# Kernel tuning notes

Hardware: AMD Instinct MI355X
Metric: run time of the kernel (lower is better)

## Reference

```python
import jax, jax.numpy as jnp
import numpy as np

B = 8
A = 180      # num_angles
D = 512      # det_count
IMG = 512    # img_size


def _forward(x):
    # --- Ram-Lak filter in frequency domain ---
    freq = jnp.abs(jnp.fft.rfftfreq(D)).astype(jnp.float32)            # [D//2+1]
    filtered = jnp.fft.irfft(jnp.fft.rfft(x, axis=-1) * freq, n=D, axis=-1)  # [B,A,D]

    # --- precompute per-angle detector coordinates for every pixel ---
    lin = jnp.linspace(-1.0, 1.0, IMG, dtype=jnp.float32)
    yy, xx = jnp.meshgrid(lin, lin, indexing='ij')
    xxf = xx.reshape(-1)                                               # [HW]
    yyf = yy.reshape(-1)
    angles = jnp.linspace(0.0, np.pi - np.pi / A, A, dtype=jnp.float32)
    t = (xxf[None, :] * jnp.cos(angles)[:, None]
         + yyf[None, :] * jnp.sin(angles)[:, None]) / np.sqrt(2.0)     # [A,HW]
    u = jnp.clip((t + 1.0) * 0.5 * (D - 1.0), 0.0, D - 1.0)
    idx0 = jnp.floor(u).astype(jnp.int32)
    idx1 = jnp.minimum(idx0 + 1, D - 1)
    w = u - idx0.astype(jnp.float32)

    # --- backprojection sweep: scan over angles, accumulate in-register ---
    proj = jnp.transpose(filtered, (1, 0, 2))                          # [A,B,D]

    def step(acc, inputs):
        p, i0, i1, wa = inputs                                         # p:[B,D], i*/wa:[HW]
        s = jnp.take(p, i0, axis=1) * (1.0 - wa) + jnp.take(p, i1, axis=1) * wa
        return acc + s, None

    bn = x.shape[0]
    acc0 = jnp.zeros((bn, IMG * IMG), dtype=jnp.float32)
    acc, _ = jax.lax.scan(step, acc0, (proj, idx0, idx1, w))

    det_pixel_size = 2.0 / float(D)
    fbp = acc.reshape(bn, 1, IMG, IMG) * (det_pixel_size * np.pi / float(A))

    # --- 3x3 gaussian blur (sigma=0.5), depthwise on single channel ---
    coords = jnp.arange(-1, 2, dtype=jnp.float32)
    k1 = jnp.exp(-0.5 * (coords / 0.5) ** 2)
    k1 = k1 / k1.sum()
    k2 = jnp.outer(k1, k1)[None, None]                                 # [1,1,3,3] OIHW
    fbp = jax.lax.conv_general_dilated(fbp, k2, (1, 1), 'SAME')
    return jnp.clip(fbp, -1.0, 1.0)


def setup_inputs() -> dict:
    key = jax.random.key(0)
    x = jax.random.normal(key, (B, A, D), dtype=jnp.float32)
    return {"x": x, "input_is_sinogram": 1}


def reference(x, input_is_sinogram):
    # input_is_sinogram is a constant flag (True path): x is the sinogram [B,A,D].
    return _forward(x)
```

## Files before the change

kernel.cpp:

```cpp
#include <hip/hip_runtime.h>
#include <hip/hip_fp16.h>
#include <math.h>

#define NDET 512
#define NANG 180
#define NB   8
#define NIMG 512

#define WS_CASA 0
#define WS_CBT  360
#define WS_FGA  46440
#define WS_FGB  (46440 + 368640)
#define WS_BP   (46440 + 737280)

typedef _Float16 h2_t __attribute__((ext_vector_type(2)));

__device__ __forceinline__ void gld_lds16(const void* g, void* l) {
    __builtin_amdgcn_global_load_lds((__attribute__((address_space(1))) void*)g,
                                     (__attribute__((address_space(3))) void*)l,
                                     16, 0, 0);
}

__device__ __forceinline__ int hswz(int s) {
    return (s & 0x78) | ((s ^ (s >> 3)) & 7);
}

__global__ __launch_bounds__(512) void k_filter(const float* __restrict__ x, float* ws) {
    __shared__ float xs[8 * 516];
    __shared__ float hrs[512];
    __shared__ float fsm[512 * 8];
    const int a    = blockIdx.x;
    const int tid  = threadIdx.x;
    const int lane = tid & 63;
    const int wv   = tid >> 6;

    {
        int n = tid;
        float h;
        if (n == 0) h = 0.25f;
        else if ((n & 1) == 0) h = 0.0f;
        else {
            int m = min(n, 512 - n);
            float s = __sinf((float)m * (float)(M_PI / 512.0));
            h = -1.0f / (262144.0f * s * s);
        }
        hrs[hswz(n >> 2) * 4 + (n & 3)] = h;
    }
    {
        const float* xr = x + (wv * NANG + a) * NDET;
        float* xd = xs + wv * 516;
        *(float4*)(xd + lane * 4)       = *(const float4*)(xr + lane * 4);
        *(float4*)(xd + 256 + lane * 4) = *(const float4*)(xr + 256 + lane * 4);
    }
    if (tid == 0) {
        double th = (double)a * (M_PI / 180.0);
        double sc = 255.5 / sqrt(2.0);
        ws[WS_CASA + 2 * a]     = (float)(cos(th) * sc);
        ws[WS_CASA + 2 * a + 1] = (float)(sin(th) * sc);
    }
    if (tid < 256) {
        double th = (double)a * (M_PI / 180.0);
        double sc = 255.5 / sqrt(2.0);
        const float cad = (float)(cos(th) * sc), sad = (float)(sin(th) * sc);
        const int bx = tid & 15, by = tid >> 4;
        const float x0 = -1.f + (float)(bx * 32)      * (2.f / 511.f);
        const float x1 = -1.f + (float)(bx * 32 + 31) * (2.f / 511.f);
        const float y0 = -1.f + (float)(by * 32)      * (2.f / 511.f);
        const float y1 = -1.f + (float)(by * 32 + 31) * (2.f / 511.f);
        float u00 = fmaf(x0, cad, fmaf(y0, sad, 255.5f));
        float u01 = fmaf(x1, cad, fmaf(y0, sad, 255.5f));
        float u10 = fmaf(x0, cad, fmaf(y1, sad, 255.5f));
        float u11 = fmaf(x1, cad, fmaf(y1, sad, 255.5f));
        float umin = fminf(fminf(u00, u01), fminf(u10, u11));
        int d0 = (int)floorf(umin);
        d0 = max(0, min(NDET - 34, d0));
        ws[WS_CBT + tid * 180 + a] = 255.5f - (float)d0;
    }
    __syncthreads();

    {
        const int b  = lane & 7;
        const int t  = lane >> 3;
        const int n0 = wv * 64 + t * 8;
        const int q  = n0 >> 2;
        const float* xrow = xs + b * 516;

        float acc[8] = {0, 0, 0, 0, 0, 0, 0, 0};
        float win[12];
        {
            int s2 = (-q - 2) & 127;
            int s1 = (-q - 1) & 127;
            float4 h2 = *(const float4*)(hrs + hswz(s2) * 4);
            float4 h1 = *(const float4*)(hrs + hswz(s1) * 4);
            win[0] = h2.x; win[1] = h2.y; win[2]  = h2.z; win[3]  = h2.w;
            win[4] = h1.x; win[5] = h1.y; win[6]  = h1.z; win[7]  = h1.w;
        }
        #pragma unroll 2
        for (int c = 0; c < 128; ++c) {
            int s = (c - q) & 127;
            float4 hc = *(const float4*)(hrs + hswz(s) * 4);
            win[8] = hc.x; win[9] = hc.y; win[10] = hc.z; win[11] = hc.w;
            float4 xv = *(const float4*)(xrow + c * 4);
            float xa[4] = {xv.x, xv.y, xv.z, xv.w};
            #pragma unroll
            for (int k = 0; k < 8; ++k)
                #pragma unroll
                for (int j = 0; j < 4; ++j)
                    acc[k] = fmaf(xa[j], win[8 + j - k], acc[k]);
            #pragma unroll
            for (int i2 = 0; i2 < 8; ++i2) win[i2] = win[i2 + 4];
        }
        #pragma unroll
        for (int k = 0; k < 8; ++k)
            fsm[(n0 + k) * 8 + b] = acc[k];
    }
    __syncthreads();
    {
        const int d  = tid;
        const int d1 = min(d + 1, NDET - 1);
        const float* A  = fsm + d * 8;
        const float* Bv = fsm + d1 * 8;
        uint4 eA, eB;
        unsigned wds[8];
        #pragma unroll
        for (int b = 0; b < 8; ++b) {
            __half2 h;
            h.x = __float2half(A[b]);
            h.y = __float2half(Bv[b]);
            wds[b] = __builtin_bit_cast(unsigned, h);
        }
        eA.x = wds[0]; eA.y = wds[1]; eA.z = wds[2]; eA.w = wds[3];
        eB.x = wds[4]; eB.y = wds[5]; eB.z = wds[6]; eB.w = wds[7];
        *(uint4*)((char*)(ws + WS_FGA) + (a * NDET + d) * 16) = eA;
        *(uint4*)((char*)(ws + WS_FGB) + (a * NDET + d) * 16) = eB;
    }
}

#define WWE  33
#define CHA  60
#define ECH  (CHA * WWE)

__global__ __launch_bounds__(1024, 4) void k_bp(float* ws) {
    __shared__ uint4 win4[2][2 * ECH];
    __shared__ float casal[2 * NANG];
    __shared__ float cbl[NANG];
    const int tid  = threadIdx.x;
    const int wv   = tid >> 6, lane = tid & 63;
    const int tile = blockIdx.x;
    const int bx   = tile & 15, by = tile >> 4;
    const int iy   = by * 32 + (wv >> 2) * 8 + (lane >> 3);
    const int ix   = bx * 32 + (wv & 3) * 8 + (lane & 7);
    const float xf = -1.0f + (float)ix * (2.0f / 511.0f);
    const float yf = -1.0f + (float)iy * (2.0f / 511.0f);

    const char* __restrict__ fga = (const char*)(ws + WS_FGA);
    const char* __restrict__ fgb = (const char*)(ws + WS_FGB);

    if (tid < NANG) {
        cbl[tid] = ws[WS_CBT + tile * 180 + tid];
        casal[2 * tid]     = ws[WS_CASA + 2 * tid];
        casal[2 * tid + 1] = ws[WS_CASA + 2 * tid + 1];
    }
    __syncthreads();

    auto stageq = [&](int buf, int ch) {
        #pragma unroll
        for (int r = 0; r < 4; ++r) {
            int c = r * 1024 + tid;
            if (c < 2 * ECH) {
                int reg = c / ECH;
                int e   = c - reg * ECH;
                int a   = e / 33;
                int o   = e - a * 33;
                int ag  = ch * CHA + a;
                int d0  = (int)(255.5f - cbl[ag]);
                const char* g = (reg ? fgb : fga) + (ag * NDET + d0 + o) * 16;
                gld_lds16(g, (char*)(&win4[buf][0]) + c * 16);
            }
        }
    };

    float acc[8] = {0, 0, 0, 0, 0, 0, 0, 0};
    auto comp = [&](int buf, int ch) {
        #pragma unroll 4
        for (int al = 0; al < CHA; ++al) {
            const int ag = ch * CHA + al;
            const float ca = casal[2 * ag], sa = casal[2 * ag + 1];
            const float cb = cbl[ag];
            float v = fmaf(xf, ca, fmaf(yf, sa, cb));
            v = __builtin_amdgcn_fmed3f(v, 0.0f, 32.99996948f);
            float fj = floorf(v);
            float w  = v - fj;
            int  j0  = (int)fj;
            uint4 dA = win4[buf][al * WWE + j0];
            uint4 dB = win4[buf][ECH + al * WWE + j0];
            h2_t wp = __builtin_bit_cast(h2_t, __builtin_amdgcn_cvt_pkrtz(1.0f - w, w));
            acc[0] = __builtin_amdgcn_fdot2(__builtin_bit_cast(h2_t, dA.x), wp, acc[0], false);
            acc[1] = __builtin_amdgcn_fdot2(__builtin_bit_cast(h2_t, dA.y), wp, acc[1], false);
            acc[2] = __builtin_amdgcn_fdot2(__builtin_bit_cast(h2_t, dA.z), wp, acc[2], false);
            acc[3] = __builtin_amdgcn_fdot2(__builtin_bit_cast(h2_t, dA.w), wp, acc[3], false);
            acc[4] = __builtin_amdgcn_fdot2(__builtin_bit_cast(h2_t, dB.x), wp, acc[4], false);
            acc[5] = __builtin_amdgcn_fdot2(__builtin_bit_cast(h2_t, dB.y), wp, acc[5], false);
            acc[6] = __builtin_amdgcn_fdot2(__builtin_bit_cast(h2_t, dB.z), wp, acc[6], false);
            acc[7] = __builtin_amdgcn_fdot2(__builtin_bit_cast(h2_t, dB.w), wp, acc[7], false);
        }
    };

    stageq(0, 0); __syncthreads();
    stageq(1, 1); comp(0, 0); __syncthreads();
    stageq(0, 2); comp(1, 1); __syncthreads();
    comp(0, 2);

    const float scale = (float)((2.0 / 512.0) * M_PI / 180.0);
    float* bp = ws + WS_BP;
    #pragma unroll
    for (int b = 0; b < 8; ++b)
        bp[b * (NIMG * NIMG) + iy * NIMG + ix] = acc[b] * scale;
}

__global__ __launch_bounds__(256) void k_blur(const float* __restrict__ ws, float* __restrict__ out) {
    const int gid = blockIdx.x * 256 + threadIdx.x;
    const int b  = gid >> 18;
    const int r  = (gid >> 9) & 511;
    const int cx = gid & 511;
    const float KA = 0.10650697891920077f;
    const float KB = 0.78698604216159850f;
    const float* img = ws + WS_BP + b * (NIMG * NIMG);
    const float* rp = img + r * 512 + cx;

    float rowm = 0.0f, row0, rowp = 0.0f;
    {
        float l  = (cx > 0)   ? rp[-1] : 0.0f;
        float rr = (cx < 511) ? rp[1]  : 0.0f;
        row0 = KA * (l + rr) + KB * rp[0];
    }
    if (r > 0) {
        const float* q = rp - 512;
        float l  = (cx > 0)   ? q[-1] : 0.0f;
        float rr = (cx < 511) ? q[1]  : 0.0f;
        rowm = KA * (l + rr) + KB * q[0];
    }
    if (r < 511) {
        const float* q = rp + 512;
        float l  = (cx > 0)   ? q[-1] : 0.0f;
        float rr = (cx < 511) ? q[1]  : 0.0f;
        rowp = KA * (l + rr) + KB * q[0];
    }
    float v = KA * (rowm + rowp) + KB * row0;
    v = fminf(fmaxf(v, -1.0f), 1.0f);
    out[gid] = v;
}

extern "C" void kernel_launch(void* const* d_in, const int* in_sizes, int n_in,
                              void* d_out, int out_size, void* d_ws, size_t ws_size,
                              hipStream_t stream) {
    const float* x = (const float*)d_in[0];
    float* out = (float*)d_out;
    float* ws  = (float*)d_ws;

    k_filter<<<NANG, 512, 0, stream>>>(x, ws);
    k_bp<<<256, 1024, 0, stream>>>(ws);
    k_blur<<<(NB * NIMG * NIMG) / 256, 256, 0, stream>>>(ws, out);
}
```

Measured before the change: 67.05 us.

## Fuse Gaussian blur into backprojection kernel using halo tiles in LDS

Each backprojection block now computes a 34x34 tile including a one-pixel halo, then performs the 3x3 blur and clamp from shared memory and writes the final output directly. This removes the separate blur kernel launch and the full-image intermediate write and read through the workspace. In exchange, roughly 13% extra pixels are backprojected and a subset of threads run a second compute pass, lengthening the per-block critical path. Detector window width grows by one to cover the halo.

```diff
diff --git a/kernel.cpp b/kernel.cpp
--- a/kernel.cpp
+++ b/kernel.cpp
@@ -11,7 +11,6 @@
 #define WS_CBT  360
 #define WS_FGA  46440
 #define WS_FGB  (46440 + 368640)
-#define WS_BP   (46440 + 737280)
 
 typedef _Float16 h2_t __attribute__((ext_vector_type(2)));
 
@@ -63,17 +62,17 @@
         double sc = 255.5 / sqrt(2.0);
         const float cad = (float)(cos(th) * sc), sad = (float)(sin(th) * sc);
         const int bx = tid & 15, by = tid >> 4;
-        const float x0 = -1.f + (float)(bx * 32)      * (2.f / 511.f);
-        const float x1 = -1.f + (float)(bx * 32 + 31) * (2.f / 511.f);
-        const float y0 = -1.f + (float)(by * 32)      * (2.f / 511.f);
-        const float y1 = -1.f + (float)(by * 32 + 31) * (2.f / 511.f);
+        const float x0 = -1.f + (float)(bx * 32 - 1)  * (2.f / 511.f);
+        const float x1 = -1.f + (float)(bx * 32 + 32) * (2.f / 511.f);
+        const float y0 = -1.f + (float)(by * 32 - 1)  * (2.f / 511.f);
+        const float y1 = -1.f + (float)(by * 32 + 32) * (2.f / 511.f);
         float u00 = fmaf(x0, cad, fmaf(y0, sad, 255.5f));
         float u01 = fmaf(x1, cad, fmaf(y0, sad, 255.5f));
         float u10 = fmaf(x0, cad, fmaf(y1, sad, 255.5f));
         float u11 = fmaf(x1, cad, fmaf(y1, sad, 255.5f));
         float umin = fminf(fminf(u00, u01), fminf(u10, u11));
         int d0 = (int)floorf(umin);
-        d0 = max(0, min(NDET - 34, d0));
+        d0 = max(0, min(NDET - 35, d0));
         ws[WS_CBT + tid * 180 + a] = 255.5f - (float)d0;
     }
     __syncthreads();
@@ -136,22 +135,30 @@
     }
 }
 
-#define WWE  33
+#define WWE  34
 #define CHA  60
 #define ECH  (CHA * WWE)
 
-__global__ __launch_bounds__(1024, 4) void k_bp(float* ws) {
+__global__ __launch_bounds__(1024, 4) void k_bp(float* ws, float* __restrict__ out) {
     __shared__ uint4 win4[2][2 * ECH];
     __shared__ float casal[2 * NANG];
     __shared__ float cbl[NANG];
     const int tid  = threadIdx.x;
-    const int wv   = tid >> 6, lane = tid & 63;
     const int tile = blockIdx.x;
     const int bx   = tile & 15, by = tile >> 4;
-    const int iy   = by * 32 + (wv >> 2) * 8 + (lane >> 3);
-    const int ix   = bx * 32 + (wv & 3) * 8 + (lane & 7);
-    const float xf = -1.0f + (float)ix * (2.0f / 511.0f);
-    const float yf = -1.0f + (float)iy * (2.0f / 511.0f);
+
+    const int lx1 = tid % 34, ly1 = tid / 34;
+    const int lp2 = 1024 + tid;
+    const int lx2 = lp2 % 34, ly2 = lp2 / 34;
+    const bool has2 = (tid < 132);
+    const int gx1 = bx * 32 - 1 + lx1, gy1 = by * 32 - 1 + ly1;
+    const int gx2 = bx * 32 - 1 + lx2, gy2 = by * 32 - 1 + ly2;
+    const bool in1 = (gx1 >= 0) && (gx1 < NIMG) && (gy1 >= 0) && (gy1 < NIMG);
+    const bool in2 = has2 && (gx2 >= 0) && (gx2 < NIMG) && (gy2 >= 0) && (gy2 < NIMG);
+    const float xf1 = -1.0f + (float)gx1 * (2.0f / 511.0f);
+    const float yf1 = -1.0f + (float)gy1 * (2.0f / 511.0f);
+    const float xf2 = -1.0f + (float)gx2 * (2.0f / 511.0f);
+    const float yf2 = -1.0f + (float)gy2 * (2.0f / 511.0f);
 
     const char* __restrict__ fga = (const char*)(ws + WS_FGA);
     const char* __restrict__ fgb = (const char*)(ws + WS_FGB);
@@ -170,8 +177,8 @@
             if (c < 2 * ECH) {
                 int reg = c / ECH;
                 int e   = c - reg * ECH;
-                int a   = e / 33;
-                int o   = e - a * 33;
+                int a   = e / WWE;
+                int o   = e - a * WWE;
                 int ag  = ch * CHA + a;
                 int d0  = (int)(255.5f - cbl[ag]);
                 const char* g = (reg ? fgb : fga) + (ag * NDET + d0 + o) * 16;
@@ -180,15 +187,16 @@
         }
     };
 
-    float acc[8] = {0, 0, 0, 0, 0, 0, 0, 0};
-    auto comp = [&](int buf, int ch) {
+    float acc1[8] = {0, 0, 0, 0, 0, 0, 0, 0};
+    float acc2[8] = {0, 0, 0, 0, 0, 0, 0, 0};
+    auto comp = [&](int buf, int ch, float xf, float yf, float* acc) {
         #pragma unroll 4
         for (int al = 0; al < CHA; ++al) {
             const int ag = ch * CHA + al;
             const float ca = casal[2 * ag], sa = casal[2 * ag + 1];
             const float cb = cbl[ag];
             float v = fmaf(xf, ca, fmaf(yf, sa, cb));
-            v = __builtin_amdgcn_fmed3f(v, 0.0f, 32.99996948f);
+            v = __builtin_amdgcn_fmed3f(v, 0.0f, 33.99996948f);
             float fj = floorf(v);
             float w  = v - fj;
             int  j0  = (int)fj;
@@ -207,48 +215,40 @@
     };
 
     stageq(0, 0); __syncthreads();
-    stageq(1, 1); comp(0, 0); __syncthreads();
-    stageq(0, 2); comp(1, 1); __syncthreads();
-    comp(0, 2);
+    stageq(1, 1);
+    comp(0, 0, xf1, yf1, acc1);
+    if (has2) comp(0, 0, xf2, yf2, acc2);
+    __syncthreads();
+    stageq(0, 2);
+    comp(1, 1, xf1, yf1, acc1);
+    if (has2) comp(1, 1, xf2, yf2, acc2);
+    __syncthreads();
+    comp(0, 2, xf1, yf1, acc1);
+    if (has2) comp(0, 2, xf2, yf2, acc2);
 
     const float scale = (float)((2.0 / 512.0) * M_PI / 180.0);
-    float* bp = ws + WS_BP;
-    #pragma unroll
-    for (int b = 0; b < 8; ++b)
-        bp[b * (NIMG * NIMG) + iy * NIMG + ix] = acc[b] * scale;
-}
-
-__global__ __launch_bounds__(256) void k_blur(const float* __restrict__ ws, float* __restrict__ out) {
-    const int gid = blockIdx.x * 256 + threadIdx.x;
-    const int b  = gid >> 18;
-    const int r  = (gid >> 9) & 511;
-    const int cx = gid & 511;
     const float KA = 0.10650697891920077f;
     const float KB = 0.78698604216159850f;
-    const float* img = ws + WS_BP + b * (NIMG * NIMG);
-    const float* rp = img + r * 512 + cx;
-
-    float rowm = 0.0f, row0, rowp = 0.0f;
-    {
-        float l  = (cx > 0)   ? rp[-1] : 0.0f;
-        float rr = (cx < 511) ? rp[1]  : 0.0f;
-        row0 = KA * (l + rr) + KB * rp[0];
-    }
-    if (r > 0) {
-        const float* q = rp - 512;
-        float l  = (cx > 0)   ? q[-1] : 0.0f;
-        float rr = (cx < 511) ? q[1]  : 0.0f;
-        rowm = KA * (l + rr) + KB * q[0];
-    }
-    if (r < 511) {
-        const float* q = rp + 512;
-        float l  = (cx > 0)   ? q[-1] : 0.0f;
-        float rr = (cx < 511) ? q[1]  : 0.0f;
-        rowp = KA * (l + rr) + KB * q[0];
-    }
-    float v = KA * (rowm + rowp) + KB * row0;
-    v = fminf(fmaxf(v, -1.0f), 1.0f);
-    out[gid] = v;
+    float* grid = (float*)&win4[0][0];
+    const int ixl = (tid & 31) + 1, iyl = (tid >> 5) + 1;
+    const int ogx = bx * 32 + (tid & 31), ogy = by * 32 + (tid >> 5);
+
+    #pragma unroll
+    for (int b = 0; b < 8; ++b) {
+        __syncthreads();
+        grid[ly1 * 35 + lx1] = in1 ? acc1[b] * scale : 0.0f;
+        if (has2) grid[ly2 * 35 + lx2] = in2 ? acc2[b] * scale : 0.0f;
+        __syncthreads();
+        const float* g0 = grid + (iyl - 1) * 35 + ixl;
+        const float* g1 = grid + iyl * 35 + ixl;
+        const float* g2 = grid + (iyl + 1) * 35 + ixl;
+        float rowm = KA * (g0[-1] + g0[1]) + KB * g0[0];
+        float row0 = KA * (g1[-1] + g1[1]) + KB * g1[0];
+        float rowp = KA * (g2[-1] + g2[1]) + KB * g2[0];
+        float v = KA * (rowm + rowp) + KB * row0;
+        v = fminf(fmaxf(v, -1.0f), 1.0f);
+        out[b * (NIMG * NIMG) + ogy * NIMG + ogx] = v;
+    }
 }
 
 extern "C" void kernel_launch(void* const* d_in, const int* in_sizes, int n_in,
@@ -259,6 +259,5 @@
     float* ws  = (float*)d_ws;
 
     k_filter<<<NANG, 512, 0, stream>>>(x, ws);
-    k_bp<<<256, 1024, 0, stream>>>(ws);
-    k_blur<<<(NB * NIMG * NIMG) / 256, 256, 0, stream>>>(ws, out);
-}
+    k_bp<<<256, 1024, 0, stream>>>(ws, out);
+}
```

Result: faster. 64.63 us (-3.6%).
